# Optimization experiments

Hardware: AMD Instinct MI355X
Metric: run time of the kernel (lower is better)

Reference implementation:

```python
import jax, jax.numpy as jnp
import numpy as np

T, F, H = 2048, 256, 384  # seq_len, input_size, hidden_size


def setup_inputs() -> dict:
    key = jax.random.key(0)
    ks = jax.random.split(key, 16)
    s = 1.0 / np.sqrt(F)
    d = {"x": jax.random.normal(ks[0], (T, F), jnp.float32)}
    names = ["q", "k", "v", "i", "f", "o"]
    for j, n in enumerate(names):
        d[f"W{n}"] = jax.random.uniform(ks[1 + j], (H, F), jnp.float32, -s, s)
        d[f"b{n}"] = jax.random.uniform(ks[7 + j], (H,), jnp.float32, -s, s)
    d["conv_w"] = jax.random.uniform(ks[13], (1, 1, 4), jnp.float32, -0.5, 0.5)
    d["conv_b"] = jax.random.uniform(ks[14], (1,), jnp.float32, -0.5, 0.5)
    return d


def _forward(x, Wq, bq, Wk, bk, Wv, bv, Wi, bi, Wf, bf, Wo, bo, conv_w, conv_b):
    # Conv1d(1->1, kernel=4, padding=(3,3)) along time, per input feature.
    xt = x.T[:, None, :]  # (F, 1, T)  feature axis acts as batch
    y = jax.lax.conv_general_dilated(xt, conv_w, (1,), [(3, 3)])  # (F, 1, T+3)
    xp = (y[:, 0, :] + conv_b[0]).T  # (T+3, F)

    inv_sqrt_h = 1.0 / jnp.sqrt(jnp.asarray(H, xp.dtype))
    # Precompute all per-step projections with dense GEMMs (time-parallel part).
    q = xp @ Wq.T + bq                      # (T+3, H)
    k = (xp @ Wk.T + bk) * inv_sqrt_h       # (T+3, H); extra bias_k is zero-init
    v = xp @ Wv.T + bv
    i = jnp.exp(xp @ Wi.T + bi)
    f = jax.nn.sigmoid(xp @ Wf.T + bf)
    o = jax.nn.sigmoid(xp @ Wo.T + bo)

    def step(carry, inp):
        C, n = carry                         # C: (H,H), n: (H,)
        qt, kt, vt, it, ft, ot = inp
        C = ft * C + it * jnp.outer(vt, kt)  # broadcast over last axis, as original
        n = ft * n + it * kt
        den = jnp.maximum(jnp.abs(jnp.dot(n, qt)), 1.0)
        h = ot * (C @ qt) / den
        return (C, n), h

    init = (jnp.zeros((H, H), xp.dtype), jnp.zeros((H,), xp.dtype))
    _, hs = jax.lax.scan(step, init, (q, k, v, i, f, o))
    return hs[-1]  # return_all=False -> last hidden state, shape (H,)


def reference(x, Wq, bq, Wk, bk, Wv, bv, Wi, bi, Wf, bf, Wo, bo, conv_w, conv_b):
    return _forward(x, Wq, bq, Wk, bk, Wv, bv, Wi, bi, Wf, bf, Wo, bo, conv_w, conv_b)
```

## Files before the change

kernel.cpp:

```cpp
#include <hip/hip_runtime.h>
#include <math.h>

#define T_IN 2048
#define TP   2051
#define F    256
#define H    384
#define XTS  2112
#define NT4  33
#define NBP  12
#define NCS  257
#define NC3  257

typedef __attribute__((ext_vector_type(8))) float float8;

__device__ __forceinline__ float logsig(float z) {
    return (z >= 0.0f) ? -log1pf(__expf(-z)) : z - log1pf(__expf(z));
}

__global__ __launch_bounds__(256) void k1_front(const float* __restrict__ x,
        const float* __restrict__ cw, const float* __restrict__ cb,
        const float* __restrict__ Wq, const float* __restrict__ bq,
        const float* __restrict__ Wo, const float* __restrict__ bo,
        float* __restrict__ xp, float* __restrict__ xpT,
        float* __restrict__ q, float* __restrict__ o,
        float* __restrict__ zf) {
    int bid = blockIdx.x;
    int tid = threadIdx.x;
    if (bid < 513) {
        __shared__ float tr[4][257];
        int tl = tid >> 6;
        int f4 = tid & 63;
        int t = bid * 4 + tl;
        float4 acc = {0.f, 0.f, 0.f, 0.f};
        if (t < TP) {
            float w[4] = {cw[0], cw[1], cw[2], cw[3]};
            float b = cb[0];
            acc.x = b; acc.y = b; acc.z = b; acc.w = b;
            int i0 = t - 3;
            const float4* x4 = (const float4*)x;
            #pragma unroll
            for (int j = 0; j < 4; ++j) {
                int tt = i0 + j;
                if (tt >= 0 && tt < T_IN) {
                    float4 xv = x4[tt * 64 + f4];
                    acc.x = fmaf(w[j], xv.x, acc.x);
                    acc.y = fmaf(w[j], xv.y, acc.y);
                    acc.z = fmaf(w[j], xv.z, acc.z);
                    acc.w = fmaf(w[j], xv.w, acc.w);
                }
            }
            ((float4*)xp)[t * 64 + f4] = acc;
        }
        *(float4*)&tr[tl][f4 * 4] = acc;
        __syncthreads();
        float4 v;
        v.x = tr[0][tid]; v.y = tr[1][tid]; v.z = tr[2][tid]; v.w = tr[3][tid];
        *(float4*)&xpT[tid * XTS + bid * 4] = v;
    } else if (bid < 609) {
        int lane = tid & 63;
        int row = (bid - 513) * 4 + (tid >> 6);
        float w0 = cw[0], b = cb[0];
        float4 xr = ((const float4*)x)[2047 * 64 + lane];
        float4 xv;
        xv.x = fmaf(w0, xr.x, b);
        xv.y = fmaf(w0, xr.y, b);
        xv.z = fmaf(w0, xr.z, b);
        xv.w = fmaf(w0, xr.w, b);
        float4 q4 = *(const float4*)&Wq[row * 256 + lane * 4];
        float4 o4 = *(const float4*)&Wo[row * 256 + lane * 4];
        float aq = fmaf(xv.x, q4.x, fmaf(xv.y, q4.y, fmaf(xv.z, q4.z, xv.w * q4.w)));
        float ao = fmaf(xv.x, o4.x, fmaf(xv.y, o4.y, fmaf(xv.z, o4.z, xv.w * o4.w)));
        #pragma unroll
        for (int off = 32; off; off >>= 1) {
            aq += __shfl_down(aq, off, 64);
            ao += __shfl_down(ao, off, 64);
        }
        if (lane == 0) {
            q[row] = aq + bq[row];
            o[row] = 1.0f / (1.0f + __expf(-(ao + bo[row])));
        }
    } else {
        for (int i = tid; i < 272; i += 256) zf[i] = 0.0f;
        for (int i = tid; i < 256 * 60; i += 256) {
            int r = i / 60, c = 2052 + i % 60;
            xpT[r * XTS + c] = 0.0f;
        }
    }
}

__global__ __launch_bounds__(256) void k2_proj(
    const float* __restrict__ xpT,
    const float* __restrict__ Wk, const float* __restrict__ bk,
    const float* __restrict__ Wi, const float* __restrict__ bi,
    const float* __restrict__ Wf, const float* __restrict__ bf,
    float* __restrict__ zk, float* __restrict__ ai, float* __restrict__ lf,
    float* __restrict__ cs) {
    __shared__ float als[2][8][64];
    __shared__ float st[32][65];
    int tid = threadIdx.x;
    int lane = tid & 63;
    int wv = __builtin_amdgcn_readfirstlane(tid >> 6);
    int mz = blockIdx.z;
    const float* __restrict__ W    = (mz == 0) ? Wk : (mz == 1) ? Wi : Wf;
    const float* __restrict__ bias = (mz == 0) ? bk : (mz == 1) ? bi : bf;
    int t0 = blockIdx.x * 64, p0 = blockIdx.y * 32;
    const float* __restrict__ Wb = W + (p0 + wv * 8) * 256;

    float acc[8];
    #pragma unroll
    for (int r = 0; r < 8; ++r) acc[r] = 0.f;

    int kr = tid >> 5;
    int tq = (tid & 31) * 2;
    const float* ap = &xpT[kr * XTS + t0 + tq];
    float2 areg = *(const float2*)ap;

    for (int kt = 0; kt < 32; ++kt) {
        int buf = kt & 1;
        *(float2*)&als[buf][kr][tq] = areg;
        float8 wr0 = *(const float8*)&Wb[0 * 256 + kt * 8];
        float8 wr1 = *(const float8*)&Wb[1 * 256 + kt * 8];
        float8 wr2 = *(const float8*)&Wb[2 * 256 + kt * 8];
        float8 wr3 = *(const float8*)&Wb[3 * 256 + kt * 8];
        float8 wr4 = *(const float8*)&Wb[4 * 256 + kt * 8];
        float8 wr5 = *(const float8*)&Wb[5 * 256 + kt * 8];
        float8 wr6 = *(const float8*)&Wb[6 * 256 + kt * 8];
        float8 wr7 = *(const float8*)&Wb[7 * 256 + kt * 8];
        __syncthreads();
        if (kt < 31) areg = *(const float2*)(ap + (kt + 1) * 8 * XTS);
        #pragma unroll
        for (int j = 0; j < 8; ++j) {
            float a = als[buf][j][lane];
            acc[0] = fmaf(wr0[j], a, acc[0]);
            acc[1] = fmaf(wr1[j], a, acc[1]);
            acc[2] = fmaf(wr2[j], a, acc[2]);
            acc[3] = fmaf(wr3[j], a, acc[3]);
            acc[4] = fmaf(wr4[j], a, acc[4]);
            acc[5] = fmaf(wr5[j], a, acc[5]);
            acc[6] = fmaf(wr6[j], a, acc[6]);
            acc[7] = fmaf(wr7[j], a, acc[7]);
        }
    }
    const float sc = 0.05103103630798287f;
    __syncthreads();
    #pragma unroll
    for (int r = 0; r < 8; ++r) {
        float v = acc[r] + bias[p0 + wv * 8 + r];
        if (mz == 0) v *= sc;
        else if (mz == 2) v = logsig(v);
        st[wv * 8 + r][lane] = v;
    }
    __syncthreads();
    float* __restrict__ OUT = (mz == 0) ? zk : (mz == 1) ? ai : lf;
    {
        int tloc = tid >> 2;
        int bq = (tid & 3) * 8;
        int t = t0 + tloc;
        if (t < TP) {
            float4 v0, v1;
            v0.x = st[bq + 0][tloc]; v0.y = st[bq + 1][tloc];
            v0.z = st[bq + 2][tloc]; v0.w = st[bq + 3][tloc];
            v1.x = st[bq + 4][tloc]; v1.y = st[bq + 5][tloc];
            v1.z = st[bq + 6][tloc]; v1.w = st[bq + 7][tloc];
            *(float4*)&OUT[t * H + p0 + bq] = v0;
            *(float4*)&OUT[t * H + p0 + bq + 4] = v1;
        }
    }
    if (mz == 2) {
        int b_l = tid & 31;
        int ch = tid >> 5;
        int c = blockIdx.x * 8 + ch;
        if (c < NCS) {
            float s = 0.f;
            #pragma unroll
            for (int j = 0; j < 8; ++j) {
                int t = t0 + ch * 8 + j;
                if (t < TP) s += st[b_l][ch * 8 + j];
            }
            cs[c * H + p0 + b_l] = s;
        }
    }
}

__global__ __launch_bounds__(64) void k3b_scan(const float* __restrict__ cs,
                                               float* __restrict__ co) {
    int b = blockIdx.x * 64 + threadIdx.x;
    float L = 0.0f;
    #pragma unroll 16
    for (int c = NCS - 1; c >= 0; --c) {
        co[c * H + b] = L;
        L += cs[c * H + b];
    }
}

__global__ __launch_bounds__(384) void k3_fused(
    const float* __restrict__ ai, const float* __restrict__ lf,
    const float* __restrict__ zk, const float* __restrict__ co,
    const float* __restrict__ q, const float* __restrict__ xp,
    float* __restrict__ zf, float* __restrict__ Gf) {
    __shared__ float zred[6][256];
    __shared__ float gred[6];
    int tid = threadIdx.x;
    int w = tid >> 6, lane = tid & 63;
    int c = blockIdx.x, ts = c * 8;
    float co0 = co[c * H + tid];
    float qb = q[tid];
    float aiv[8], lfv[8], zkv[8];
    float4 xv[8];
    if (ts + 8 <= TP) {
        #pragma unroll
        for (int u = 0; u < 8; ++u) {
            int idx = (ts + u) * H + tid;
            aiv[u] = ai[idx]; lfv[u] = lf[idx]; zkv[u] = zk[idx];
            xv[u] = *(const float4*)&xp[(ts + u) * 256 + lane * 4];
        }
    } else {
        #pragma unroll
        for (int u = 0; u < 8; ++u) {
            if (ts + u < TP) {
                int idx = (ts + u) * H + tid;
                aiv[u] = ai[idx]; lfv[u] = lf[idx]; zkv[u] = zk[idx];
                xv[u] = *(const float4*)&xp[(ts + u) * 256 + lane * 4];
            } else {
                aiv[u] = -1e30f; lfv[u] = 0.f; zkv[u] = 0.f;
                xv[u].x = xv[u].y = xv[u].z = xv[u].w = 0.f;
            }
        }
    }
    float S = 0.f, gsum = 0.f;
    float z0 = 0.f, z1 = 0.f, z2 = 0.f, z3 = 0.f;
    #pragma unroll
    for (int u = 7; u >= 0; --u) {
        float wv = __expf(aiv[u] + co0 + S) * zkv[u] * qb;
        S += lfv[u];
        float s = wv;
        s += __shfl_xor(s, 1, 64);
        s += __shfl_xor(s, 2, 64);
        s += __shfl_xor(s, 4, 64);
        s += __shfl_xor(s, 8, 64);
        s += __shfl_xor(s, 16, 64);
        s += __shfl_xor(s, 32, 64);
        gsum += s;
        z0 = fmaf(s, xv[u].x, z0);
        z1 = fmaf(s, xv[u].y, z1);
        z2 = fmaf(s, xv[u].z, z2);
        z3 = fmaf(s, xv[u].w, z3);
    }
    zred[w][lane * 4 + 0] = z0;
    zred[w][lane * 4 + 1] = z1;
    zred[w][lane * 4 + 2] = z2;
    zred[w][lane * 4 + 3] = z3;
    if (lane == 0) gred[w] = gsum;
    __syncthreads();
    if (tid < 256) {
        float s = zred[0][tid] + zred[1][tid] + zred[2][tid]
                + zred[3][tid] + zred[4][tid] + zred[5][tid];
        atomicAdd(&zf[tid], s);
    }
    if (tid == 0)
        atomicAdd(Gf, gred[0] + gred[1] + gred[2] + gred[3] + gred[4] + gred[5]);
}

__global__ __launch_bounds__(256) void k6_out(const float* __restrict__ zf,
        const float* __restrict__ Gf,
        const float* __restrict__ Wv, const float* __restrict__ bv,
        const float* __restrict__ o, float* __restrict__ out) {
    int tid = threadIdx.x;
    int lane = tid & 63;
    int row = blockIdx.x * 4 + (tid >> 6);
    float Gv = Gf[0];
    float4 zv = *(const float4*)&zf[lane * 4];
    float4 wv = *(const float4*)&Wv[row * 256 + lane * 4];
    float acc = fmaf(zv.x, wv.x, fmaf(zv.y, wv.y, fmaf(zv.z, wv.z, zv.w * wv.w)));
    #pragma unroll
    for (int off = 32; off; off >>= 1) acc += __shfl_down(acc, off, 64);
    if (lane == 0)
        out[row] = o[row] * (acc + bv[row] * Gv) / fmaxf(fabsf(Gv), 1.0f);
}

extern "C" void kernel_launch(void* const* d_in, const int* in_sizes, int n_in,
                              void* d_out, int out_size, void* d_ws, size_t ws_size,
                              hipStream_t stream) {
    const float* x  = (const float*)d_in[0];
    const float* Wq = (const float*)d_in[1];  const float* bq = (const float*)d_in[2];
    const float* Wk = (const float*)d_in[3];  const float* bk = (const float*)d_in[4];
    const float* Wv = (const float*)d_in[5];  const float* bv = (const float*)d_in[6];
    const float* Wi = (const float*)d_in[7];  const float* bi = (const float*)d_in[8];
    const float* Wf = (const float*)d_in[9];  const float* bf = (const float*)d_in[10];
    const float* Wo = (const float*)d_in[11]; const float* bo = (const float*)d_in[12];
    const float* cw = (const float*)d_in[13]; const float* cb = (const float*)d_in[14];
    float* out = (float*)d_out;

    float* ws = (float*)d_ws;
    float* xp  = ws;
    float* zk  = xp  + TP * F;
    float* ai  = zk  + TP * H;
    float* lf  = ai  + TP * H;
    float* cs  = lf  + TP * H;
    float* co  = cs  + NCS * H;
    float* qv  = co  + NCS * H;
    float* ov  = qv  + H;
    float* zf  = ov  + H;
    float* Gf  = zf  + F;
    float* xpT = zf  + 512;

    k1_front<<<610, 256, 0, stream>>>(x, cw, cb, Wq, bq, Wo, bo, xp, xpT, qv, ov, zf);
    k2_proj<<<dim3(NT4, NBP, 3), 256, 0, stream>>>(xpT, Wk, bk, Wi, bi, Wf, bf, zk, ai, lf, cs);
    k3b_scan<<<6, 64, 0, stream>>>(cs, co);
    k3_fused<<<NC3, 384, 0, stream>>>(ai, lf, zk, co, qv, xp, zf, Gf);
    k6_out<<<96, 256, 0, stream>>>(zf, Gf, Wv, bv, ov, out);
}
```

Measured before the change: 150.2 us.

## Restructure projection GEMM into LDS-tiled 8x8 register blocking sharing activations

The k/i/f projection kernel is rewritten so that one block computes all three projections for a 64-time by 64-hidden tile, with one wave per weight matrix. Both the activation tile and the weight tiles are staged in double-buffered LDS, and each thread accumulates an 8x8 register block. This cuts redundant global loads of activations across the three matrices and raises arithmetic intensity compared with the old one-row-per-lane scheme. In exchange the grid shrinks from about 1188 blocks to 198, which lowers occupancy and parallelism, and the transposed scalar LDS writes of weights may cause bank conflicts.

```diff
diff --git a/kernel.cpp b/kernel.cpp
--- a/kernel.cpp
+++ b/kernel.cpp
@@ -6,16 +6,16 @@
 #define F    256
 #define H    384
 #define XTS  2112
-#define NT4  33
-#define NBP  12
+#define NTB  33
 #define NCS  257
 #define NC3  257
 
-typedef __attribute__((ext_vector_type(8))) float float8;
 
 __device__ __forceinline__ float logsig(float z) {
     return (z >= 0.0f) ? -log1pf(__expf(-z)) : z - log1pf(__expf(z));
 }
+
+union F4 { float4 v; float f[4]; };
 
 __global__ __launch_bounds__(256) void k1_front(const float* __restrict__ x,
         const float* __restrict__ cw, const float* __restrict__ cb,
@@ -88,96 +88,173 @@
     }
 }
 
-__global__ __launch_bounds__(256) void k2_proj(
+__global__ __launch_bounds__(192) void k2_proj(
     const float* __restrict__ xpT,
     const float* __restrict__ Wk, const float* __restrict__ bk,
     const float* __restrict__ Wi, const float* __restrict__ bi,
     const float* __restrict__ Wf, const float* __restrict__ bf,
     float* __restrict__ zk, float* __restrict__ ai, float* __restrict__ lf,
     float* __restrict__ cs) {
-    __shared__ float als[2][8][64];
-    __shared__ float st[32][65];
+    __shared__ float alds[2][32][68];
+    __shared__ float wlds[2][3][32][68];
     int tid = threadIdx.x;
+    int wv = tid >> 6;
     int lane = tid & 63;
-    int wv = __builtin_amdgcn_readfirstlane(tid >> 6);
-    int mz = blockIdx.z;
-    const float* __restrict__ W    = (mz == 0) ? Wk : (mz == 1) ? Wi : Wf;
-    const float* __restrict__ bias = (mz == 0) ? bk : (mz == 1) ? bi : bf;
-    int t0 = blockIdx.x * 64, p0 = blockIdx.y * 32;
-    const float* __restrict__ Wb = W + (p0 + wv * 8) * 256;
-
-    float acc[8];
-    #pragma unroll
-    for (int r = 0; r < 8; ++r) acc[r] = 0.f;
-
-    int kr = tid >> 5;
-    int tq = (tid & 31) * 2;
-    const float* ap = &xpT[kr * XTS + t0 + tq];
-    float2 areg = *(const float2*)ap;
-
-    for (int kt = 0; kt < 32; ++kt) {
-        int buf = kt & 1;
-        *(float2*)&als[buf][kr][tq] = areg;
-        float8 wr0 = *(const float8*)&Wb[0 * 256 + kt * 8];
-        float8 wr1 = *(const float8*)&Wb[1 * 256 + kt * 8];
-        float8 wr2 = *(const float8*)&Wb[2 * 256 + kt * 8];
-        float8 wr3 = *(const float8*)&Wb[3 * 256 + kt * 8];
-        float8 wr4 = *(const float8*)&Wb[4 * 256 + kt * 8];
-        float8 wr5 = *(const float8*)&Wb[5 * 256 + kt * 8];
-        float8 wr6 = *(const float8*)&Wb[6 * 256 + kt * 8];
-        float8 wr7 = *(const float8*)&Wb[7 * 256 + kt * 8];
+    int tg = lane >> 3;
+    int bg = lane & 7;
+    int t0 = blockIdx.x * 64, b0 = blockIdx.y * 64;
+    const float* __restrict__ bias = (wv == 0) ? bk : (wv == 1) ? bi : bf;
+
+    float4 accA[8], accB[8];
+    #pragma unroll
+    for (int i = 0; i < 8; ++i) {
+        accA[i].x = accA[i].y = accA[i].z = accA[i].w = 0.f;
+        accB[i].x = accB[i].y = accB[i].z = accB[i].w = 0.f;
+    }
+
+    float4 awp[3], wwp[8];
+    #pragma unroll
+    for (int r = 0; r < 3; ++r) {
+        int j = tid + r * 192;
+        if (j < 512) {
+            int k = j >> 4, t4 = (j & 15) * 4;
+            awp[r] = *(const float4*)&xpT[k * XTS + t0 + t4];
+        }
+    }
+    #pragma unroll
+    for (int r = 0; r < 8; ++r) {
+        int fl = tid + r * 192;
+        int m = fl >> 9, rem = fl & 511;
+        int b = rem >> 3, kq = (rem & 7) * 4;
+        const float* Wm = (m == 0) ? Wk : (m == 1) ? Wi : Wf;
+        wwp[r] = *(const float4*)&Wm[(b0 + b) * 256 + kq];
+    }
+
+    for (int it = 0; it < 8; ++it) {
+        int buf = it & 1;
+        #pragma unroll
+        for (int r = 0; r < 3; ++r) {
+            int j = tid + r * 192;
+            if (j < 512) {
+                int k = j >> 4, t4 = (j & 15) * 4;
+                *(float4*)&alds[buf][k][t4] = awp[r];
+            }
+        }
+        #pragma unroll
+        for (int r = 0; r < 8; ++r) {
+            int fl = tid + r * 192;
+            int m = fl >> 9, rem = fl & 511;
+            int b = rem >> 3, kq = (rem & 7) * 4;
+            F4 u; u.v = wwp[r];
+            #pragma unroll
+            for (int j = 0; j < 4; ++j)
+                wlds[buf][m][kq + j][b] = u.f[j];
+        }
         __syncthreads();
-        if (kt < 31) areg = *(const float2*)(ap + (kt + 1) * 8 * XTS);
-        #pragma unroll
-        for (int j = 0; j < 8; ++j) {
-            float a = als[buf][j][lane];
-            acc[0] = fmaf(wr0[j], a, acc[0]);
-            acc[1] = fmaf(wr1[j], a, acc[1]);
-            acc[2] = fmaf(wr2[j], a, acc[2]);
-            acc[3] = fmaf(wr3[j], a, acc[3]);
-            acc[4] = fmaf(wr4[j], a, acc[4]);
-            acc[5] = fmaf(wr5[j], a, acc[5]);
-            acc[6] = fmaf(wr6[j], a, acc[6]);
-            acc[7] = fmaf(wr7[j], a, acc[7]);
-        }
-    }
-    const float sc = 0.05103103630798287f;
-    __syncthreads();
-    #pragma unroll
-    for (int r = 0; r < 8; ++r) {
-        float v = acc[r] + bias[p0 + wv * 8 + r];
-        if (mz == 0) v *= sc;
-        else if (mz == 2) v = logsig(v);
-        st[wv * 8 + r][lane] = v;
-    }
-    __syncthreads();
-    float* __restrict__ OUT = (mz == 0) ? zk : (mz == 1) ? ai : lf;
-    {
-        int tloc = tid >> 2;
-        int bq = (tid & 3) * 8;
-        int t = t0 + tloc;
-        if (t < TP) {
-            float4 v0, v1;
-            v0.x = st[bq + 0][tloc]; v0.y = st[bq + 1][tloc];
-            v0.z = st[bq + 2][tloc]; v0.w = st[bq + 3][tloc];
-            v1.x = st[bq + 4][tloc]; v1.y = st[bq + 5][tloc];
-            v1.z = st[bq + 6][tloc]; v1.w = st[bq + 7][tloc];
-            *(float4*)&OUT[t * H + p0 + bq] = v0;
-            *(float4*)&OUT[t * H + p0 + bq + 4] = v1;
-        }
-    }
-    if (mz == 2) {
-        int b_l = tid & 31;
-        int ch = tid >> 5;
-        int c = blockIdx.x * 8 + ch;
+        if (it < 7) {
+            int k0 = (it + 1) * 32;
+            #pragma unroll
+            for (int r = 0; r < 3; ++r) {
+                int j = tid + r * 192;
+                if (j < 512) {
+                    int k = j >> 4, t4 = (j & 15) * 4;
+                    awp[r] = *(const float4*)&xpT[(k0 + k) * XTS + t0 + t4];
+                }
+            }
+            #pragma unroll
+            for (int r = 0; r < 8; ++r) {
+                int fl = tid + r * 192;
+                int m = fl >> 9, rem = fl & 511;
+                int b = rem >> 3, kq = (rem & 7) * 4;
+                const float* Wm = (m == 0) ? Wk : (m == 1) ? Wi : Wf;
+                wwp[r] = *(const float4*)&Wm[(b0 + b) * 256 + k0 + kq];
+            }
+        }
+        #pragma unroll 4
+        for (int kk = 0; kk < 32; ++kk) {
+            F4 A0, A1, W0, W1;
+            A0.v = *(const float4*)&alds[buf][kk][tg * 8];
+            A1.v = *(const float4*)&alds[buf][kk][tg * 8 + 4];
+            W0.v = *(const float4*)&wlds[buf][wv][kk][bg * 8];
+            W1.v = *(const float4*)&wlds[buf][wv][kk][bg * 8 + 4];
+            #pragma unroll
+            for (int i = 0; i < 8; ++i) {
+                float av = (i < 4) ? A0.f[i] : A1.f[i - 4];
+                accA[i].x = fmaf(av, W0.f[0], accA[i].x);
+                accA[i].y = fmaf(av, W0.f[1], accA[i].y);
+                accA[i].z = fmaf(av, W0.f[2], accA[i].z);
+                accA[i].w = fmaf(av, W0.f[3], accA[i].w);
+                accB[i].x = fmaf(av, W1.f[0], accB[i].x);
+                accB[i].y = fmaf(av, W1.f[1], accB[i].y);
+                accB[i].z = fmaf(av, W1.f[2], accB[i].z);
+                accB[i].w = fmaf(av, W1.f[3], accB[i].w);
+            }
+        }
+        __syncthreads();
+    }
+    int bA = b0 + bg * 8;
+    float4 b4a = *(const float4*)&bias[bA];
+    float4 b4b = *(const float4*)&bias[bA + 4];
+    if (wv == 0) {
+        const float sc = 0.05103103630798287f;
+        #pragma unroll
+        for (int i = 0; i < 8; ++i) {
+            int t = t0 + tg * 8 + i;
+            if (t < TP) {
+                float4 v0, v1;
+                v0.x = (accA[i].x + b4a.x) * sc; v0.y = (accA[i].y + b4a.y) * sc;
+                v0.z = (accA[i].z + b4a.z) * sc; v0.w = (accA[i].w + b4a.w) * sc;
+                v1.x = (accB[i].x + b4b.x) * sc; v1.y = (accB[i].y + b4b.y) * sc;
+                v1.z = (accB[i].z + b4b.z) * sc; v1.w = (accB[i].w + b4b.w) * sc;
+                *(float4*)&zk[t * H + bA] = v0;
+                *(float4*)&zk[t * H + bA + 4] = v1;
+            }
+        }
+    } else if (wv == 1) {
+        #pragma unroll
+        for (int i = 0; i < 8; ++i) {
+            int t = t0 + tg * 8 + i;
+            if (t < TP) {
+                float4 v0, v1;
+                v0.x = accA[i].x + b4a.x; v0.y = accA[i].y + b4a.y;
+                v0.z = accA[i].z + b4a.z; v0.w = accA[i].w + b4a.w;
+                v1.x = accB[i].x + b4b.x; v1.y = accB[i].y + b4b.y;
+                v1.z = accB[i].z + b4b.z; v1.w = accB[i].w + b4b.w;
+                *(float4*)&ai[t * H + bA] = v0;
+                *(float4*)&ai[t * H + bA + 4] = v1;
+            }
+        }
+    } else {
+        float4 s0a = {0,0,0,0}, s0b = {0,0,0,0}, s1a = {0,0,0,0}, s1b = {0,0,0,0};
+        #pragma unroll
+        for (int i = 0; i < 8; ++i) {
+            int t = t0 + tg * 8 + i;
+            if (t < TP) {
+                float4 l0, l1;
+                l0.x = logsig(accA[i].x + b4a.x); l0.y = logsig(accA[i].y + b4a.y);
+                l0.z = logsig(accA[i].z + b4a.z); l0.w = logsig(accA[i].w + b4a.w);
+                l1.x = logsig(accB[i].x + b4b.x); l1.y = logsig(accB[i].y + b4b.y);
+                l1.z = logsig(accB[i].z + b4b.z); l1.w = logsig(accB[i].w + b4b.w);
+                *(float4*)&lf[t * H + bA] = l0;
+                *(float4*)&lf[t * H + bA + 4] = l1;
+                if (i < 4) {
+                    s0a.x += l0.x; s0a.y += l0.y; s0a.z += l0.z; s0a.w += l0.w;
+                    s0b.x += l1.x; s0b.y += l1.y; s0b.z += l1.z; s0b.w += l1.w;
+                } else {
+                    s1a.x += l0.x; s1a.y += l0.y; s1a.z += l0.z; s1a.w += l0.w;
+                    s1b.x += l1.x; s1b.y += l1.y; s1b.z += l1.z; s1b.w += l1.w;
+                }
+            }
+        }
+        int c = blockIdx.x * 8 + tg;
         if (c < NCS) {
-            float s = 0.f;
-            #pragma unroll
-            for (int j = 0; j < 8; ++j) {
-                int t = t0 + ch * 8 + j;
-                if (t < TP) s += st[b_l][ch * 8 + j];
-            }
-            cs[c * H + p0 + b_l] = s;
+            float4 c0, c1;
+            c0.x = s0a.x + s1a.x; c0.y = s0a.y + s1a.y;
+            c0.z = s0a.z + s1a.z; c0.w = s0a.w + s1a.w;
+            c1.x = s0b.x + s1b.x; c1.y = s0b.y + s1b.y;
+            c1.z = s0b.z + s1b.z; c1.w = s0b.w + s1b.w;
+            *(float4*)&cs[c * H + bA] = c0;
+            *(float4*)&cs[c * H + bA + 4] = c1;
         }
     }
 }
@@ -305,7 +382,7 @@
     float* xpT = zf  + 512;
 
     k1_front<<<610, 256, 0, stream>>>(x, cw, cb, Wq, bq, Wo, bo, xp, xpT, qv, ov, zf);
-    k2_proj<<<dim3(NT4, NBP, 3), 256, 0, stream>>>(xpT, Wk, bk, Wi, bi, Wf, bf, zk, ai, lf, cs);
+    k2_proj<<<dim3(NTB, 6), 192, 0, stream>>>(xpT, Wk, bk, Wi, bi, Wf, bf, zk, ai, lf, cs);
     k3b_scan<<<6, 64, 0, stream>>>(cs, co);
     k3_fused<<<NC3, 384, 0, stream>>>(ai, lf, zk, co, qv, xp, zf, Gf);
     k6_out<<<96, 256, 0, stream>>>(zf, Gf, Wv, bv, ov, out);
```

Result: slower. 314.9 us (+109.6%).
